# Performance work log

Measured on AMD Instinct MI355X. Metric: run time of the kernel, lower is better.

The kernel has to match this reference:

```python
import jax, jax.numpy as jnp
import numpy as np

B, L, D, W = 4, 256, 256, 8  # batch, seq_len, d_model, context_window
NS_EPS = 1e-7


def setup_inputs() -> dict:
    key = jax.random.key(0)
    ks = jax.random.split(key, 12)
    f = lambda k, s: jax.random.normal(k, s, dtype=jnp.float32)
    sD = 1.0 / np.sqrt(D)
    return {
        "x": f(ks[0], (B, L, D)),
        "k_aligned": jnp.tanh(f(ks[1], (B, L, D))),  # QKProjectionLayer applies tanh upstream
        "v": f(ks[2], (B, L, D)),
        "M_prev": f(ks[3], (B, D, D)) * 0.01,
        "S_prev": jnp.zeros((B, D, D), jnp.float32),
        # polynomial feature coeffs: phi(k) = c1*k + c2*k^2 (degree 2, dim-preserving)
        "poly_coeffs": jnp.stack([jnp.ones((D,), jnp.float32), 0.1 * jnp.ones((D,), jnp.float32)])
        + 0.01 * f(ks[4], (2, D)),
        "alpha_W": f(ks[5], (D, D)) * sD, "alpha_b": jnp.zeros((D,), jnp.float32),
        "eta_W": f(ks[6], (D, D)) * sD, "eta_b": jnp.zeros((D,), jnp.float32),
        "theta_W": f(ks[7], (D, D)) * sD, "theta_b": jnp.zeros((D,), jnp.float32),
        "gamma_W": f(ks[8], (D,)) * sD, "gamma_b": jnp.zeros((1,), jnp.float32),
        "out_W": f(ks[9], (D, D)) * sD, "out_b": jnp.zeros((D,), jnp.float32),
    }


def _newton_schulz_1(S):
    # NS_K with K=1: X <- 1.5*X - 0.5*X X^T X after Frobenius normalization
    norm = jnp.sqrt(jnp.sum(S * S, axis=(-2, -1), keepdims=True)) + NS_EPS
    X = S / norm
    return 1.5 * X - 0.5 * jnp.einsum('bij,bkj,bkl->bil', X, X, X)


def reference(x, k_aligned, v, M_prev, S_prev, poly_coeffs,
              alpha_W, alpha_b, eta_W, eta_b, theta_W, theta_b,
              gamma_W, gamma_b, out_W, out_b):
    Bn, Ln, Dn = x.shape
    # polynomial feature layer (dim-preserving, degree 2)
    k_phi = poly_coeffs[0] * k_aligned + poly_coeffs[1] * k_aligned ** 2  # [B,L,D]
    # per-token gates (precomputed, pure linear+sigmoid)
    alpha = jax.nn.sigmoid(x @ alpha_W.T + alpha_b)          # [B,L,D]
    eta = jax.nn.sigmoid(x @ eta_W.T + eta_b) * 0.1          # [B,L,D]
    theta = jax.nn.sigmoid(x @ theta_W.T + theta_b)          # [B,L,D]
    gamma = jax.nn.sigmoid(jnp.einsum('bld,d->bl', x, gamma_W) + gamma_b[0])  # [B,L]
    c_arr = jnp.minimum(jnp.arange(Ln) + 1, W).astype(x.dtype)  # actual window length per step

    to_t = lambda a: jnp.moveaxis(a, 1, 0)  # [B,L,...] -> [L,B,...]
    xs = (to_t(k_phi), to_t(v), to_t(gamma), to_t(alpha), to_t(eta), to_t(theta), c_arr)

    buf_k = jnp.zeros((Bn, W, Dn), x.dtype)  # sliding window of phi(k); zero pads contribute 0
    buf_v = jnp.zeros((Bn, W, Dn), x.dtype)
    buf_g = jnp.zeros((Bn, W), x.dtype)

    def step(carry, xt):
        M, S, bk, bv, bg = carry
        k_t, v_t, g_t, a_t, e_t, th_t, c_t = xt
        bk = jnp.concatenate([bk[:, 1:], k_t[:, None]], axis=1)
        bv = jnp.concatenate([bv[:, 1:], v_t[:, None]], axis=1)
        bg = jnp.concatenate([bg[:, 1:], g_t[:, None]], axis=1)
        # Omega gradient: sum_i gamma_i * (M phi(k_i) - v_i) outer phi(k_i) / c
        pred = jnp.einsum('bde,bwe->bwd', M, bk)
        err = pred - bv
        grad = jnp.einsum('bw,bwd,bwe->bde', bg, err, bk) / c_t
        S = th_t[..., None] * S + grad
        S_ortho = _newton_schulz_1(S)
        M = a_t[..., None] * M - e_t[..., None] * S_ortho
        y = jnp.einsum('bde,be->bd', M, k_t)
        return (M, S, bk, bv, bg), y

    (M, S, _, _, _), ys = jax.lax.scan(step, (M_prev, S_prev, buf_k, buf_v, buf_g), xs)
    output = jnp.moveaxis(ys, 0, 1) @ out_W.T + out_b  # out_proj per token
    return (output, M, S)
```

## Files before the change

### kernel.cpp

```cpp
#include <hip/hip_runtime.h>

#define Bn 4
#define Ln 256
#define Dn 256
#define Wn 8
#define NBLK 64
#define BLD (Bn*Ln*Dn)
#define BDD (Bn*Dn*Dn)

typedef float  floatx4 __attribute__((ext_vector_type(4)));
typedef short  short8  __attribute__((ext_vector_type(8)));

__device__ __forceinline__ float ldc(const float* p) {
    return __hip_atomic_load(p, __ATOMIC_RELAXED, __HIP_MEMORY_SCOPE_AGENT);
}
__device__ __forceinline__ void stc(float* p, float v) {
    __hip_atomic_store(p, v, __ATOMIC_RELAXED, __HIP_MEMORY_SCOPE_AGENT);
}
__device__ __forceinline__ void stc4(float* p, floatx4 v) {
    asm volatile("global_store_dwordx4 %0, %1, off sc0 sc1" :: "v"(p), "v"(v) : "memory");
}
__device__ __forceinline__ void ldc1x4(float& a, float& b, float& c, float& d,
    const float* p0, const float* p1, const float* p2, const float* p3)
{
    asm volatile(
        "global_load_dword %0, %4, off sc0 sc1\n\t"
        "global_load_dword %1, %5, off sc0 sc1\n\t"
        "global_load_dword %2, %6, off sc0 sc1\n\t"
        "global_load_dword %3, %7, off sc0 sc1\n\t"
        "s_waitcnt vmcnt(0)"
        : "=&v"(a), "=&v"(b), "=&v"(c), "=&v"(d)
        : "v"(p0), "v"(p1), "v"(p2), "v"(p3)
        : "memory");
}
__device__ __forceinline__ void ldc4x12s(
    floatx4& r0, floatx4& r1, floatx4& r2, floatx4& r3,
    floatx4& r4, floatx4& r5, floatx4& r6, floatx4& r7,
    floatx4& r8, floatx4& r9, floatx4& r10, floatx4& r11, float& sc,
    const float* p0, const float* p1, const float* p2, const float* p3,
    const float* p4, const float* p5, const float* p6, const float* p7,
    const float* p8, const float* p9, const float* p10, const float* p11,
    const float* ps)
{
    asm volatile(
        "global_load_dwordx4 %0, %13, off sc0 sc1\n\t"
        "global_load_dwordx4 %1, %14, off sc0 sc1\n\t"
        "global_load_dwordx4 %2, %15, off sc0 sc1\n\t"
        "global_load_dwordx4 %3, %16, off sc0 sc1\n\t"
        "global_load_dwordx4 %4, %17, off sc0 sc1\n\t"
        "global_load_dwordx4 %5, %18, off sc0 sc1\n\t"
        "global_load_dwordx4 %6, %19, off sc0 sc1\n\t"
        "global_load_dwordx4 %7, %20, off sc0 sc1\n\t"
        "global_load_dwordx4 %8, %21, off sc0 sc1\n\t"
        "global_load_dwordx4 %9, %22, off sc0 sc1\n\t"
        "global_load_dwordx4 %10, %23, off sc0 sc1\n\t"
        "global_load_dwordx4 %11, %24, off sc0 sc1\n\t"
        "global_load_dword %12, %25, off sc0 sc1\n\t"
        "s_waitcnt vmcnt(0)"
        : "=&v"(r0), "=&v"(r1), "=&v"(r2), "=&v"(r3),
          "=&v"(r4), "=&v"(r5), "=&v"(r6), "=&v"(r7),
          "=&v"(r8), "=&v"(r9), "=&v"(r10), "=&v"(r11), "=&v"(sc)
        : "v"(p0), "v"(p1), "v"(p2), "v"(p3), "v"(p4), "v"(p5),
          "v"(p6), "v"(p7), "v"(p8), "v"(p9), "v"(p10), "v"(p11), "v"(ps)
        : "memory");
}

__device__ __forceinline__ unsigned f2bf(float x) {
    unsigned u = __float_as_uint(x);
    return (u + 0x7FFFu + ((u >> 16) & 1u)) >> 16;
}
__device__ __forceinline__ unsigned long long packbf4(floatx4 v) {
    unsigned lo = f2bf(v[0]) | (f2bf(v[1]) << 16);
    unsigned hi = f2bf(v[2]) | (f2bf(v[3]) << 16);
    return (unsigned long long)lo | ((unsigned long long)hi << 32);
}
union BF8 { short8 s8; unsigned long long u[2]; };

__device__ __forceinline__ void grid_sync_b(unsigned* bflags, int rem, unsigned k)
{
    asm volatile("s_waitcnt vmcnt(0) lgkmcnt(0)" ::: "memory");
    __syncthreads();
    if (threadIdx.x == 0)
        __hip_atomic_store(&bflags[rem * 32], k,
                           __ATOMIC_RELAXED, __HIP_MEMORY_SCOPE_AGENT);
    if (threadIdx.x < 16) {
        while (__hip_atomic_load(&bflags[threadIdx.x * 32],
                                 __ATOMIC_RELAXED, __HIP_MEMORY_SCOPE_AGENT) < k)
            __builtin_amdgcn_s_sleep(1);
    }
    __syncthreads();
}

__global__ __launch_bounds__(256) void kphi_gamma_kernel(
    const float* __restrict__ k_al, const float* __restrict__ x,
    const float* __restrict__ poly, const float* __restrict__ gW,
    const float* __restrict__ gb, float* __restrict__ kphi,
    float* __restrict__ gamma)
{
    int wg = blockIdx.x, tid = threadIdx.x;
    int wave = tid >> 6, lane = tid & 63;
    int n = wg * 4 + wave;
    float gacc = 0.f;
#pragma unroll
    for (int c = 0; c < 4; ++c) {
        int e = lane + 64 * c;
        float kv = k_al[n * Dn + e];
        kphi[n * Dn + e] = poly[e] * kv + poly[Dn + e] * kv * kv;
        gacc += x[n * Dn + e] * gW[e];
    }
#pragma unroll
    for (int off = 32; off; off >>= 1) gacc += __shfl_xor(gacc, off);
    if (lane == 0) gamma[n] = 1.f / (1.f + expf(-(gacc + gb[0])));
}

template <int ACT>
__global__ __launch_bounds__(256) void gemm_act_kernel(
    const float* __restrict__ In, const float* __restrict__ Wm,
    const float* __restrict__ bias, float* __restrict__ Out)
{
    __shared__ float ldsX[32 * 64];
    __shared__ float ldsW[64 * 65];
    int n0 = blockIdx.x * 32;
    int m0 = blockIdx.y * 64;
    int tid = threadIdx.x;
    float acc[8] = {0, 0, 0, 0, 0, 0, 0, 0};
    for (int j0 = 0; j0 < 256; j0 += 64) {
#pragma unroll
        for (int q = 0; q < 2; ++q) {
            int fi = tid + 256 * q; int row = fi >> 4; int c4 = (fi & 15) << 2;
            *(float4*)&ldsX[row * 64 + c4] =
                *(const float4*)&In[(n0 + row) * 256 + j0 + c4];
        }
#pragma unroll
        for (int q = 0; q < 4; ++q) {
            int fi = tid + 256 * q; int row = fi >> 4; int c4 = (fi & 15) << 2;
            float4 vv = *(const float4*)&Wm[(m0 + row) * 256 + j0 + c4];
            ldsW[(c4 + 0) * 65 + row] = vv.x;
            ldsW[(c4 + 1) * 65 + row] = vv.y;
            ldsW[(c4 + 2) * 65 + row] = vv.z;
            ldsW[(c4 + 3) * 65 + row] = vv.w;
        }
        __syncthreads();
        int m = tid & 63, ng = tid >> 6;
        for (int j = 0; j < 64; ++j) {
            float wv = ldsW[j * 65 + m];
#pragma unroll
            for (int r = 0; r < 8; ++r) acc[r] += ldsX[(ng * 8 + r) * 64 + j] * wv;
        }
        __syncthreads();
    }
    int m = tid & 63, ng = tid >> 6;
    float bv = bias[m0 + m];
#pragma unroll
    for (int r = 0; r < 8; ++r) {
        float vv = acc[r] + bv;
        if (ACT == 1) vv = 1.f / (1.f + expf(-vv));
        if (ACT == 2) vv = 0.1f / (1.f + expf(-vv));
        Out[(n0 + ng * 8 + r) * 256 + m0 + m] = vv;
    }
}

__global__ __launch_bounds__(64) void kgram_kernel(
    const float* __restrict__ kphi, float* __restrict__ Kall)
{
    int t = blockIdx.x, b = blockIdx.y, tid = threadIdx.x;
    int wa = tid >> 3, wb = tid & 7;
    int ta = t - 7 + wa, tb = t - 7 + wb;
    float g = 0.f;
    if (ta >= 0 && tb >= 0) {
        const float* pa = &kphi[(b * Ln + ta) * Dn];
        const float* pb = &kphi[(b * Ln + tb) * Dn];
        for (int j = 0; j < Dn; j += 4) {
            floatx4 x1 = *(const floatx4*)&pa[j];
            floatx4 x2 = *(const floatx4*)&pb[j];
            g += x1[0]*x2[0] + x1[1]*x2[1] + x1[2]*x2[2] + x1[3]*x2[3];
        }
    }
    Kall[(b * Ln + t) * 64 + tid] = g;
}

__global__ __launch_bounds__(256) void prologue_kernel(unsigned* __restrict__ flags)
{
    int gidx = blockIdx.x * 256 + threadIdx.x;
    if (gidx < 512) {
        uint4 zu = {0u, 0u, 0u, 0u};
        ((uint4*)flags)[gidx] = zu;
    }
}

__global__ __launch_bounds__(256) void ysum_kernel(float* __restrict__ ysp)
{
    int gidx = blockIdx.x * 256 + threadIdx.x;
    float4 a = ((float4*)ysp)[gidx];
    float4 b = ((float4*)ysp)[65536 + gidx];
    float4 c = ((float4*)ysp)[131072 + gidx];
    float4 d = ((float4*)ysp)[196608 + gidx];
    a.x += b.x + c.x + d.x;
    a.y += b.y + c.y + d.y;
    a.z += b.z + c.z + d.z;
    a.w += b.w + c.w + d.w;
    ((float4*)ysp)[gidx] = a;
}

#define OFF_ST    0
#define OFF_UV    8448
#define OFF_AV    10496
#define OFF_CV    12544
#define OFF_TH    14592
#define OFF_KT    14848
#define OFF_KL    15104
#define OFF_NRM   15168
#define OFF_WSUM  15184
#define OFF_US    15200
#define OFF_KWA   15328
#define OFF_KW2   17408
#define OFF_SL    19456
#define SMEM_FLOATS 23616

__global__ void __launch_bounds__(256, 1) scan_kernel(
    const float* __restrict__ kphi, const float* __restrict__ vin,
    const float* __restrict__ gammaB, const float* __restrict__ alphaB,
    const float* __restrict__ etaB, const float* __restrict__ thetaB,
    const float* __restrict__ Kall,
    const float* __restrict__ Mprev, const float* __restrict__ Sprev,
    unsigned short* __restrict__ STg,
    float* __restrict__ u_buf, float* __restrict__ a_buf,
    float* __restrict__ errp_g, float* __restrict__ normp,
    float* __restrict__ ysp, unsigned* __restrict__ flags,
    float* __restrict__ outM, float* __restrict__ outS)
{
    __shared__ float smem[SMEM_FLOATS];
    char*  STb  = (char*)(smem + OFF_ST);
    float* uvp  = smem + OFF_UV;
    float* avp  = smem + OFF_AV;
    float* cvp  = smem + OFF_CV;
    float* thv  = smem + OFF_TH;
    float* kT   = smem + OFF_KT;
    float* Kl   = smem + OFF_KL;
    float* nrml = smem + OFF_NRM;
    float* wsum = smem + OFF_WSUM;
    float* usl  = smem + OFF_US;
    float* kWA  = smem + OFF_KWA;
    float* kW2  = smem + OFF_KW2;
    float* Sl   = smem + OFF_SL;

    const int wg = blockIdx.x, tid = threadIdx.x;
    const int b   = wg >> 4;
    const int rem = wg & 15;
    const int s   = rem & 3;
    const int i0 = (rem >> 2) * 64, l0 = (rem & 3) * 64;
    const int d0 = rem << 4;
    const int wid = tid >> 6, lane = tid & 63;
    const int lme = lane & 15, hi = lane >> 4;
    const int ibr = i0 + wid * 16 + (hi << 2);
    const int r  = tid >> 4, m = tid & 15;
    unsigned* bflags = flags + b * 512;
    unsigned kbar = 0;

    floatx4 S_reg[4];
    float   M_reg[16];
    floatx4 T_reg[16];

    {
#pragma unroll
        for (int cq = 0; cq < 4; ++cq)
            S_reg[cq] = *(const floatx4*)&Sprev[(size_t)(b*256 + d0 + r)*256 + m*4 + 64*cq];
#pragma unroll
        for (int lt = 0; lt < 4; ++lt)
#pragma unroll
            for (int g = 0; g < 4; ++g)
                M_reg[lt*4+g] = Mprev[(size_t)(b*256 + ibr + g)*256 + l0 + lt*16 + lme];

        float* scratch = smem;
        for (int g4 = 0; g4 < 4; ++g4) {
            floatx4 acc[4];
#pragma unroll
            for (int lt = 0; lt < 4; ++lt) acc[lt] = (floatx4){0.f,0.f,0.f,0.f};
#pragma unroll
            for (int kc = 0; kc < 8; ++kc) {
                int kb2 = kc*32 + hi*8;
                floatx4 a0 = *(const floatx4*)&Sprev[(size_t)(b*256 + i0 + wid*16 + lme)*256 + kb2];
                floatx4 a1 = *(const floatx4*)&Sprev[(size_t)(b*256 + i0 + wid*16 + lme)*256 + kb2 + 4];
                BF8 ua; ua.u[0] = packbf4(a0); ua.u[1] = packbf4(a1);
#pragma unroll
                for (int lt = 0; lt < 4; ++lt) {
                    int brow = g4*64 + lt*16 + lme;
                    floatx4 b0 = *(const floatx4*)&Sprev[(size_t)(b*256 + brow)*256 + kb2];
                    floatx4 b1 = *(const floatx4*)&Sprev[(size_t)(b*256 + brow)*256 + kb2 + 4];
                    BF8 ub; ub.u[0] = packbf4(b0); ub.u[1] = packbf4(b1);
                    acc[lt] = __builtin_amdgcn_mfma_f32_16x16x32_bf16(ua.s8, ub.s8, acc[lt], 0,0,0);
                }
            }
#pragma unroll
            for (int lt = 0; lt < 4; ++lt)
#pragma unroll
                for (int g = 0; g < 4; ++g)
                    scratch[(wid*16 + (hi<<2) + g)*260 + g4*64 + lt*16 + lme] = acc[lt][g];
        }
        __syncthreads();
#pragma unroll
        for (int kc = 0; kc < 8; ++kc) {
            T_reg[kc*2+0] = *(floatx4*)&scratch[(wid*16 + lme)*260 + kc*32 + hi*8];
            T_reg[kc*2+1] = *(floatx4*)&scratch[(wid*16 + lme)*260 + kc*32 + hi*8 + 4];
        }
#pragma unroll
        for (int q = 0; q < 2; ++q) {
            int w = q*4 + (tid >> 6);
            int c4 = (tid & 63) << 2;
            floatx4 kv = {0.f,0.f,0.f,0.f};
            if (w == 7) kv = *(const floatx4*)&kphi[(size_t)(b*Ln)*Dn + c4];
            *(floatx4*)&kW2[w*256 + c4] = kv;
        }
        __syncthreads();
#pragma unroll
        for (int w = 0; w < 8; ++w) {
            float pd[4] = {0.f,0.f,0.f,0.f};
#pragma unroll
            for (int lt = 0; lt < 4; ++lt) {
                float kv2 = kW2[w*256 + l0 + lt*16 + lme];
#pragma unroll
                for (int g = 0; g < 4; ++g) pd[g] += M_reg[lt*4+g] * kv2;
            }
#pragma unroll
            for (int g = 0; g < 4; ++g) {
                pd[g] += __shfl_xor(pd[g], 1); pd[g] += __shfl_xor(pd[g], 2);
                pd[g] += __shfl_xor(pd[g], 4); pd[g] += __shfl_xor(pd[g], 8);
            }
            if (lme == 0)
#pragma unroll
                for (int g = 0; g < 4; ++g)
                    stc(&errp_g[(size_t)((s*2 + 0)*4 + b)*2048 + w*256 + ibr + g], pd[g]);
        }
    }
    grid_sync_b(bflags, rem, ++kbar);

    for (int t = 0; t < Ln; ++t) {
        const int cwin = (t + 1 < Wn) ? (t + 1) : Wn;
        const float invc = 1.f / (float)cwin;

        {
            float e0_ = 0.f, e1_ = 0.f, e2_ = 0.f, e3_ = 0.f;
            int w_a = 0, rr_a = 0;
            const int p = t & 1;
            if (tid < 128) {
                w_a = tid >> 4; rr_a = tid & 15;
                ldc1x4(e0_, e1_, e2_, e3_,
                    &errp_g[(size_t)((0*2 + p)*4 + b)*2048 + w_a*256 + d0 + rr_a],
                    &errp_g[(size_t)((1*2 + p)*4 + b)*2048 + w_a*256 + d0 + rr_a],
                    &errp_g[(size_t)((2*2 + p)*4 + b)*2048 + w_a*256 + d0 + rr_a],
                    &errp_g[(size_t)((3*2 + p)*4 + b)*2048 + w_a*256 + d0 + rr_a]);
                float ep = e0_ + e1_ + e2_ + e3_;
                int tok = t - 7 + w_a;
                float uu = 0.f;
                if (tok >= 0)
                    uu = gammaB[b*Ln + tok] * invc *
                         (ep - vin[(size_t)(b*Ln + tok)*Dn + d0 + rr_a]);
                usl[w_a*16 + rr_a] = uu;
                stc(&u_buf[(size_t)(b*8 + w_a)*256 + d0 + rr_a], uu);
            } else {
                int idx = tid - 128;
                int w = idx >> 4, seg = idx & 15;
                int tk = t - 7 + w;
#pragma unroll
                for (int q = 0; q < 4; ++q) {
                    floatx4 kv = {0.f,0.f,0.f,0.f};
                    if (tk >= 0)
                        kv = *(const floatx4*)&kphi[(size_t)(b*Ln + tk)*Dn + seg*16 + q*4];
                    *(floatx4*)&kWA[w*260 + seg*16 + q*4] = kv;
                }
            }
            __syncthreads();

            {
                float qw[8] = {0,0,0,0,0,0,0,0};
#pragma unroll
                for (int cq = 0; cq < 4; ++cq) {
                    floatx4 sv = S_reg[cq];
#pragma unroll
                    for (int w = 0; w < 8; ++w) {
                        floatx4 kv = *(const floatx4*)&kWA[w*260 + m*4 + 64*cq];
                        qw[w] += sv[0]*kv[0] + sv[1]*kv[1] + sv[2]*kv[2] + sv[3]*kv[3];
                    }
                }
#pragma unroll
                for (int w = 0; w < 8; ++w) {
                    qw[w] += __shfl_xor(qw[w], 1); qw[w] += __shfl_xor(qw[w], 2);
                    qw[w] += __shfl_xor(qw[w], 4); qw[w] += __shfl_xor(qw[w], 8);
                }
                if (m < 8) {
                    float th = thetaB[(size_t)(b*Ln + t)*Dn + d0 + r];
                    stc(&a_buf[(size_t)(b*8 + m)*256 + d0 + r], th * qw[m]);
                }
            }
            {
                float th = thetaB[(size_t)(b*Ln + t)*Dn + d0 + r];
                float uu[8];
#pragma unroll
                for (int w = 0; w < 8; ++w) uu[w] = usl[w*16 + r];
                float sumsq = 0.f;
#pragma unroll
                for (int cq = 0; cq < 4; ++cq) {
                    floatx4 sv = th * S_reg[cq];
#pragma unroll
                    for (int w = 0; w < 8; ++w) {
                        floatx4 kv = *(const floatx4*)&kWA[w*260 + m*4 + 64*cq];
                        sv += uu[w] * kv;
                    }
                    S_reg[cq] = sv;
                    sumsq += sv[0]*sv[0] + sv[1]*sv[1] + sv[2]*sv[2] + sv[3]*sv[3];
                }
#pragma unroll
                for (int off = 32; off; off >>= 1) sumsq += __shfl_xor(sumsq, off);
                if (lane == 0) wsum[wid] = sumsq;
            }
            {
#pragma unroll
                for (int cq = 0; cq < 4; ++cq)
                    *(floatx4*)&Sl[r*260 + m*4 + 64*cq] = S_reg[cq];
                __syncthreads();
                int l = tid;
                unsigned dw[8];
#pragma unroll
                for (int j = 0; j < 8; ++j)
                    dw[j] = f2bf(Sl[(2*j)*260 + l]) | (f2bf(Sl[(2*j+1)*260 + l]) << 16);
                floatx4 p0 = { __uint_as_float(dw[0]), __uint_as_float(dw[1]),
                               __uint_as_float(dw[2]), __uint_as_float(dw[3]) };
                floatx4 p1 = { __uint_as_float(dw[4]), __uint_as_float(dw[5]),
                               __uint_as_float(dw[6]), __uint_as_float(dw[7]) };
                char* dstp = (char*)STg + ((size_t)(b*256 + l)*256 + d0)*2;
                stc4((float*)dstp, p0);
                stc4((float*)(dstp + 16), p1);
                if (tid == 0)
                    stc(&normp[b*16 + rem], wsum[0] + wsum[1] + wsum[2] + wsum[3]);
            }
            if (t == Ln - 1) {
#pragma unroll
                for (int cq = 0; cq < 4; ++cq)
                    *(floatx4*)&outS[(size_t)(b*256 + d0 + r)*256 + m*4 + 64*cq] = S_reg[cq];
            }
        }
        grid_sync_b(bflags, rem, ++kbar);

        {
            {
                int lq = tid >> 2, kq = (tid & 3) * 64;
                const char* src = (const char*)STg + ((size_t)(b*256 + l0 + lq)*256 + kq)*2;
                const float* pu = &u_buf[(size_t)b*2048 + tid*8];
                const float* pa = &a_buf[(size_t)b*2048 + tid*8];
                const float* pn = (tid < 16) ? &normp[b*16 + tid] : pu;
                floatx4 r0,r1,r2,r3,r4,r5,r6,r7,u0,u1,a0,a1; float nsc;
                ldc4x12s(r0,r1,r2,r3,r4,r5,r6,r7,u0,u1,a0,a1,nsc,
                    (const float*)(src+0),  (const float*)(src+16),
                    (const float*)(src+32), (const float*)(src+48),
                    (const float*)(src+64), (const float*)(src+80),
                    (const float*)(src+96), (const float*)(src+112),
                    pu, pu+4, pa, pa+4, pn);
                size_t rb0 = (size_t)lq*528 + (size_t)kq*2;
                unsigned swz = (unsigned)((lq & 8) << 1);
                *(floatx4*)(STb + ((rb0 +   0) ^ swz)) = r0;
                *(floatx4*)(STb + ((rb0 +  16) ^ swz)) = r1;
                *(floatx4*)(STb + ((rb0 +  32) ^ swz)) = r2;
                *(floatx4*)(STb + ((rb0 +  48) ^ swz)) = r3;
                *(floatx4*)(STb + ((rb0 +  64) ^ swz)) = r4;
                *(floatx4*)(STb + ((rb0 +  80) ^ swz)) = r5;
                *(floatx4*)(STb + ((rb0 +  96) ^ swz)) = r6;
                *(floatx4*)(STb + ((rb0 + 112) ^ swz)) = r7;
                *(floatx4*)&uvp[tid*8]     = u0; *(floatx4*)&uvp[tid*8 + 4] = u1;
                *(floatx4*)&avp[tid*8]     = a0; *(floatx4*)&avp[tid*8 + 4] = a1;
                if (tid < 16) nrml[tid] = nsc;
                if (tid < 64) {
                    *(floatx4*)&thv[tid*4] = *(const floatx4*)&thetaB[(size_t)(b*Ln + t)*Dn + tid*4];
                    *(floatx4*)&kT[tid*4]  = *(const floatx4*)&kphi[(size_t)(b*Ln + t)*Dn + tid*4];
                }
                if (tid < 16)
                    *(floatx4*)&Kl[tid*4] = *(const floatx4*)&Kall[(size_t)(b*Ln + t)*64 + tid*4];
                if (t < Ln - 1) {
#pragma unroll
                    for (int q = 0; q < 2; ++q) {
                        int w = q*4 + (tid >> 6);
                        int c4 = (tid & 63) << 2;
                        int tk = t + 1 - 7 + w;
                        floatx4 kv = {0.f,0.f,0.f,0.f};
                        if (tk >= 0) kv = *(const floatx4*)&kphi[(size_t)(b*Ln + tk)*Dn + c4];
                        *(floatx4*)&kW2[w*256 + c4] = kv;
                    }
                }
            }
            __syncthreads();

#pragma unroll
            for (int q = 0; q < 8; ++q) {
                int idx = q*256 + tid;
                int w = idx >> 8, e = idx & 255;
                float sv = avp[idx];
#pragma unroll
                for (int w2 = 0; w2 < 8; ++w2)
                    sv += 0.5f * Kl[w*8 + w2] * uvp[w2*256 + e];
                cvp[idx] = sv;
            }
            __syncthreads();

            {
                int i = i0 + wid*16 + lme;
                float thi = thv[i];
                float ui8[8], ci8[8];
#pragma unroll
                for (int w = 0; w < 8; ++w) { ui8[w] = uvp[w*256 + i]; ci8[w] = cvp[w*256 + i]; }
#pragma unroll
                for (int kc = 0; kc < 8; ++kc) {
                    int k0 = kc*32 + hi*8;
                    floatx4 th0 = *(const floatx4*)&thv[k0];
                    floatx4 th1 = *(const floatx4*)&thv[k0 + 4];
                    floatx4 t0 = (thi * th0) * T_reg[kc*2+0];
                    floatx4 t1 = (thi * th1) * T_reg[kc*2+1];
#pragma unroll
                    for (int w = 0; w < 8; ++w) {
                        floatx4 uk0 = *(const floatx4*)&uvp[w*256 + k0];
                        floatx4 uk1 = *(const floatx4*)&uvp[w*256 + k0 + 4];
                        floatx4 ck0 = *(const floatx4*)&cvp[w*256 + k0];
                        floatx4 ck1 = *(const floatx4*)&cvp[w*256 + k0 + 4];
                        t0 += ui8[w]*ck0 + ci8[w]*uk0;
                        t1 += ui8[w]*ck1 + ci8[w]*uk1;
                    }
                    T_reg[kc*2+0] = t0;
                    T_reg[kc*2+1] = t1;
                }
            }

            floatx4 acc[4];
#pragma unroll
            for (int lt = 0; lt < 4; ++lt) acc[lt] = (floatx4){0.f,0.f,0.f,0.f};
#pragma unroll
            for (int kc = 0; kc < 8; ++kc) {
                BF8 ua; ua.u[0] = packbf4(T_reg[kc*2]); ua.u[1] = packbf4(T_reg[kc*2+1]);
                int kbyte = kc*64 + hi*16;
#pragma unroll
                for (int lt = 0; lt < 4; ++lt) {
                    int row = lt*16 + lme;
                    short8 bf = *(const short8*)(STb +
                        (((size_t)row*528 + kbyte) ^ (unsigned)((row & 8) << 1)));
                    acc[lt] = __builtin_amdgcn_mfma_f32_16x16x32_bf16(ua.s8, bf, acc[lt], 0,0,0);
                }
            }

            {
                float nsq = 0.f;
#pragma unroll
                for (int q = 0; q < 16; ++q) nsq += nrml[q];
                float nrm = sqrtf(nsq) + 1e-7f;
                float inv_n = 1.f / nrm;
                float w1 = 1.5f * inv_n;
                float w3 = 0.5f * inv_n * inv_n * inv_n;
                float alv[4], etv[4], kvr[4];
#pragma unroll
                for (int g = 0; g < 4; ++g) {
                    alv[g] = alphaB[(size_t)(b*Ln + t)*Dn + ibr + g];
                    etv[g] = etaB[(size_t)(b*Ln + t)*Dn + ibr + g];
                }
#pragma unroll
                for (int lt = 0; lt < 4; ++lt) kvr[lt] = kT[l0 + lt*16 + lme];
                float py[4] = {0.f,0.f,0.f,0.f};
#pragma unroll
                for (int lt = 0; lt < 4; ++lt)
#pragma unroll
                    for (int g = 0; g < 4; ++g) {
                        int l_loc = lt*16 + lme;
                        unsigned short sb = *(const unsigned short*)(STb +
                            (((size_t)l_loc*528 + (size_t)(ibr + g)*2) ^ (unsigned)((l_loc & 8) << 1)));
                        float s_il = __uint_as_float(((unsigned)sb) << 16);
                        float ns = w1 * s_il - w3 * acc[lt][g];
                        float mn = alv[g] * M_reg[lt*4+g] - etv[g] * ns;
                        M_reg[lt*4+g] = mn;
                        py[g] += mn * kvr[lt];
                        if (t == Ln - 1)
                            outM[(size_t)(b*256 + ibr + g)*256 + l0 + l_loc] = mn;
                    }
#pragma unroll
                for (int g = 0; g < 4; ++g) {
                    py[g] += __shfl_xor(py[g], 1); py[g] += __shfl_xor(py[g], 2);
                    py[g] += __shfl_xor(py[g], 4); py[g] += __shfl_xor(py[g], 8);
                    if (lme == 0)
                        stc(&ysp[(size_t)s*BLD + (size_t)(b*Ln + t)*Dn + ibr + g], py[g]);
                }
            }

            if (t < Ln - 1) {
                const int p2 = (t + 1) & 1;
#pragma unroll
                for (int w = 0; w < 8; ++w) {
                    float pd[4] = {0.f,0.f,0.f,0.f};
#pragma unroll
                    for (int lt = 0; lt < 4; ++lt) {
                        float kv2 = kW2[w*256 + l0 + lt*16 + lme];
#pragma unroll
                        for (int g = 0; g < 4; ++g) pd[g] += M_reg[lt*4+g] * kv2;
                    }
#pragma unroll
                    for (int g = 0; g < 4; ++g) {
                        pd[g] += __shfl_xor(pd[g], 1); pd[g] += __shfl_xor(pd[g], 2);
                        pd[g] += __shfl_xor(pd[g], 4); pd[g] += __shfl_xor(pd[g], 8);
                    }
                    if (lme == 0)
#pragma unroll
                        for (int g = 0; g < 4; ++g)
                            stc(&errp_g[(size_t)((s*2 + p2)*4 + b)*2048 + w*256 + ibr + g], pd[g]);
                }
            }
        }
        grid_sync_b(bflags, rem, ++kbar);
    }
}

extern "C" void kernel_launch(void* const* d_in, const int* in_sizes, int n_in,
                              void* d_out, int out_size, void* d_ws, size_t ws_size,
                              hipStream_t stream)
{
    const float* x       = (const float*)d_in[0];
    const float* k_al    = (const float*)d_in[1];
    const float* v       = (const float*)d_in[2];
    const float* M_prev  = (const float*)d_in[3];
    const float* S_prev  = (const float*)d_in[4];
    const float* poly    = (const float*)d_in[5];
    const float* alpha_W = (const float*)d_in[6];
    const float* alpha_b = (const float*)d_in[7];
    const float* eta_W   = (const float*)d_in[8];
    const float* eta_b   = (const float*)d_in[9];
    const float* theta_W = (const float*)d_in[10];
    const float* theta_b = (const float*)d_in[11];
    const float* gamma_W = (const float*)d_in[12];
    const float* gamma_b = (const float*)d_in[13];
    const float* out_W   = (const float*)d_in[14];
    const float* out_b   = (const float*)d_in[15];

    float* ws = (float*)d_ws;
    float* kphi    = ws;
    float* alphaB  = kphi   + BLD;
    float* etaB    = alphaB + BLD;
    float* thetaB  = etaB   + BLD;
    float* gammaB  = thetaB + BLD;
    float* Kall    = gammaB + Bn*Ln;
    float* STg_f   = Kall   + Bn*Ln*64;
    float* u_bufp  = STg_f  + 131072;
    float* a_bufp  = u_bufp + Bn*Wn*Dn;
    float* errp    = a_bufp + Bn*Wn*Dn;
    float* normp   = errp   + 65536;
    float* ysp     = normp  + 64;
    unsigned* flags = (unsigned*)(ysp + 4*BLD);

    float* out_y = (float*)d_out;
    float* outM  = out_y + BLD;
    float* outS  = outM + BDD;

    hipLaunchKernelGGL(kphi_gamma_kernel, dim3(256), dim3(256), 0, stream,
                       k_al, x, poly, gamma_W, gamma_b, kphi, gammaB);
    hipLaunchKernelGGL((gemm_act_kernel<1>), dim3(32, 4), dim3(256), 0, stream,
                       x, alpha_W, alpha_b, alphaB);
    hipLaunchKernelGGL((gemm_act_kernel<2>), dim3(32, 4), dim3(256), 0, stream,
                       x, eta_W, eta_b, etaB);
    hipLaunchKernelGGL((gemm_act_kernel<1>), dim3(32, 4), dim3(256), 0, stream,
                       x, theta_W, theta_b, thetaB);
    hipLaunchKernelGGL(kgram_kernel, dim3(Ln, Bn), dim3(64), 0, stream,
                       kphi, Kall);
    hipLaunchKernelGGL(prologue_kernel, dim3(2), dim3(256), 0, stream, flags);

    hipLaunchKernelGGL(scan_kernel, dim3(NBLK), dim3(256), 0, stream,
                       kphi, v, gammaB, alphaB, etaB, thetaB, Kall,
                       M_prev, S_prev, (unsigned short*)STg_f,
                       u_bufp, a_bufp, errp, normp, ysp, flags,
                       outM, outS);

    hipLaunchKernelGGL(ysum_kernel, dim3(256), dim3(256), 0, stream, ysp);
    hipLaunchKernelGGL((gemm_act_kernel<0>), dim3(32, 4), dim3(256), 0, stream,
                       ysp, out_W, out_b, out_y);
}
```

Baseline: 5.753 ms.

## Replace persistent grid-synced scan kernel with per-timestep phase kernel launches

The single persistent scan kernel, which used spin-wait flag barriers across workgroups, is split into two kernels (phase A and phase C) launched per timestep from the host loop. Kernel boundaries now provide the synchronisation. M, S and the T matrix state live in global memory with ping-pong T buffers, and separate init kernels compute the initial T and error terms. The y partial sums are written directly, so the ysum reduction kernel is removed. This trades custom barrier overhead for 512 kernel launches and extra global memory round-trips of state.

New measurement: 5.326 ms. -7.4%, faster.

```diff
diff --git a/kernel.cpp b/kernel.cpp
--- a/kernel.cpp
+++ b/kernel.cpp
@@ -4,66 +4,11 @@
 #define Ln 256
 #define Dn 256
 #define Wn 8
-#define NBLK 64
 #define BLD (Bn*Ln*Dn)
 #define BDD (Bn*Dn*Dn)
 
 typedef float  floatx4 __attribute__((ext_vector_type(4)));
 typedef short  short8  __attribute__((ext_vector_type(8)));
-
-__device__ __forceinline__ float ldc(const float* p) {
-    return __hip_atomic_load(p, __ATOMIC_RELAXED, __HIP_MEMORY_SCOPE_AGENT);
-}
-__device__ __forceinline__ void stc(float* p, float v) {
-    __hip_atomic_store(p, v, __ATOMIC_RELAXED, __HIP_MEMORY_SCOPE_AGENT);
-}
-__device__ __forceinline__ void stc4(float* p, floatx4 v) {
-    asm volatile("global_store_dwordx4 %0, %1, off sc0 sc1" :: "v"(p), "v"(v) : "memory");
-}
-__device__ __forceinline__ void ldc1x4(float& a, float& b, float& c, float& d,
-    const float* p0, const float* p1, const float* p2, const float* p3)
-{
-    asm volatile(
-        "global_load_dword %0, %4, off sc0 sc1\n\t"
-        "global_load_dword %1, %5, off sc0 sc1\n\t"
-        "global_load_dword %2, %6, off sc0 sc1\n\t"
-        "global_load_dword %3, %7, off sc0 sc1\n\t"
-        "s_waitcnt vmcnt(0)"
-        : "=&v"(a), "=&v"(b), "=&v"(c), "=&v"(d)
-        : "v"(p0), "v"(p1), "v"(p2), "v"(p3)
-        : "memory");
-}
-__device__ __forceinline__ void ldc4x12s(
-    floatx4& r0, floatx4& r1, floatx4& r2, floatx4& r3,
-    floatx4& r4, floatx4& r5, floatx4& r6, floatx4& r7,
-    floatx4& r8, floatx4& r9, floatx4& r10, floatx4& r11, float& sc,
-    const float* p0, const float* p1, const float* p2, const float* p3,
-    const float* p4, const float* p5, const float* p6, const float* p7,
-    const float* p8, const float* p9, const float* p10, const float* p11,
-    const float* ps)
-{
-    asm volatile(
-        "global_load_dwordx4 %0, %13, off sc0 sc1\n\t"
-        "global_load_dwordx4 %1, %14, off sc0 sc1\n\t"
-        "global_load_dwordx4 %2, %15, off sc0 sc1\n\t"
-        "global_load_dwordx4 %3, %16, off sc0 sc1\n\t"
-        "global_load_dwordx4 %4, %17, off sc0 sc1\n\t"
-        "global_load_dwordx4 %5, %18, off sc0 sc1\n\t"
-        "global_load_dwordx4 %6, %19, off sc0 sc1\n\t"
-        "global_load_dwordx4 %7, %20, off sc0 sc1\n\t"
-        "global_load_dwordx4 %8, %21, off sc0 sc1\n\t"
-        "global_load_dwordx4 %9, %22, off sc0 sc1\n\t"
-        "global_load_dwordx4 %10, %23, off sc0 sc1\n\t"
-        "global_load_dwordx4 %11, %24, off sc0 sc1\n\t"
-        "global_load_dword %12, %25, off sc0 sc1\n\t"
-        "s_waitcnt vmcnt(0)"
-        : "=&v"(r0), "=&v"(r1), "=&v"(r2), "=&v"(r3),
-          "=&v"(r4), "=&v"(r5), "=&v"(r6), "=&v"(r7),
-          "=&v"(r8), "=&v"(r9), "=&v"(r10), "=&v"(r11), "=&v"(sc)
-        : "v"(p0), "v"(p1), "v"(p2), "v"(p3), "v"(p4), "v"(p5),
-          "v"(p6), "v"(p7), "v"(p8), "v"(p9), "v"(p10), "v"(p11), "v"(ps)
-        : "memory");
-}
 
 __device__ __forceinline__ unsigned f2bf(float x) {
     unsigned u = __float_as_uint(x);
@@ -75,21 +20,6 @@
     return (unsigned long long)lo | ((unsigned long long)hi << 32);
 }
 union BF8 { short8 s8; unsigned long long u[2]; };
-
-__device__ __forceinline__ void grid_sync_b(unsigned* bflags, int rem, unsigned k)
-{
-    asm volatile("s_waitcnt vmcnt(0) lgkmcnt(0)" ::: "memory");
-    __syncthreads();
-    if (threadIdx.x == 0)
-        __hip_atomic_store(&bflags[rem * 32], k,
-                           __ATOMIC_RELAXED, __HIP_MEMORY_SCOPE_AGENT);
-    if (threadIdx.x < 16) {
-        while (__hip_atomic_load(&bflags[threadIdx.x * 32],
-                                 __ATOMIC_RELAXED, __HIP_MEMORY_SCOPE_AGENT) < k)
-            __builtin_amdgcn_s_sleep(1);
-    }
-    __syncthreads();
-}
 
 __global__ __launch_bounds__(256) void kphi_gamma_kernel(
     const float* __restrict__ k_al, const float* __restrict__ x,
@@ -179,435 +109,416 @@
     Kall[(b * Ln + t) * 64 + tid] = g;
 }
 
-__global__ __launch_bounds__(256) void prologue_kernel(unsigned* __restrict__ flags)
+__global__ __launch_bounds__(256) void prologue_kernel(
+    const float* __restrict__ Mprev, const float* __restrict__ Sprev,
+    float* __restrict__ M, float* __restrict__ S,
+    float* __restrict__ ys, float* __restrict__ errp)
 {
     int gidx = blockIdx.x * 256 + threadIdx.x;
-    if (gidx < 512) {
-        uint4 zu = {0u, 0u, 0u, 0u};
-        ((uint4*)flags)[gidx] = zu;
-    }
-}
-
-__global__ __launch_bounds__(256) void ysum_kernel(float* __restrict__ ysp)
-{
-    int gidx = blockIdx.x * 256 + threadIdx.x;
-    float4 a = ((float4*)ysp)[gidx];
-    float4 b = ((float4*)ysp)[65536 + gidx];
-    float4 c = ((float4*)ysp)[131072 + gidx];
-    float4 d = ((float4*)ysp)[196608 + gidx];
-    a.x += b.x + c.x + d.x;
-    a.y += b.y + c.y + d.y;
-    a.z += b.z + c.z + d.z;
-    a.w += b.w + c.w + d.w;
-    ((float4*)ysp)[gidx] = a;
-}
-
-#define OFF_ST    0
-#define OFF_UV    8448
-#define OFF_AV    10496
-#define OFF_CV    12544
-#define OFF_TH    14592
-#define OFF_KT    14848
-#define OFF_KL    15104
-#define OFF_NRM   15168
-#define OFF_WSUM  15184
-#define OFF_US    15200
-#define OFF_KWA   15328
-#define OFF_KW2   17408
-#define OFF_SL    19456
-#define SMEM_FLOATS 23616
-
-__global__ void __launch_bounds__(256, 1) scan_kernel(
-    const float* __restrict__ kphi, const float* __restrict__ vin,
-    const float* __restrict__ gammaB, const float* __restrict__ alphaB,
-    const float* __restrict__ etaB, const float* __restrict__ thetaB,
-    const float* __restrict__ Kall,
-    const float* __restrict__ Mprev, const float* __restrict__ Sprev,
-    unsigned short* __restrict__ STg,
-    float* __restrict__ u_buf, float* __restrict__ a_buf,
-    float* __restrict__ errp_g, float* __restrict__ normp,
-    float* __restrict__ ysp, unsigned* __restrict__ flags,
-    float* __restrict__ outM, float* __restrict__ outS)
-{
-    __shared__ float smem[SMEM_FLOATS];
-    char*  STb  = (char*)(smem + OFF_ST);
-    float* uvp  = smem + OFF_UV;
-    float* avp  = smem + OFF_AV;
-    float* cvp  = smem + OFF_CV;
-    float* thv  = smem + OFF_TH;
-    float* kT   = smem + OFF_KT;
-    float* Kl   = smem + OFF_KL;
-    float* nrml = smem + OFF_NRM;
-    float* wsum = smem + OFF_WSUM;
-    float* usl  = smem + OFF_US;
-    float* kWA  = smem + OFF_KWA;
-    float* kW2  = smem + OFF_KW2;
-    float* Sl   = smem + OFF_SL;
-
+    ((float4*)M)[gidx] = ((const float4*)Mprev)[gidx];
+    ((float4*)S)[gidx] = ((const float4*)Sprev)[gidx];
+    float4 z = {0.f, 0.f, 0.f, 0.f};
+    ((float4*)ys)[gidx] = z;
+    if (gidx < 16384) ((float4*)errp)[gidx] = z;
+}
+
+__global__ __launch_bounds__(256) void tinit_kernel(
+    const float* __restrict__ Sprev, float* __restrict__ Tg0)
+{
     const int wg = blockIdx.x, tid = threadIdx.x;
-    const int b   = wg >> 4;
-    const int rem = wg & 15;
-    const int s   = rem & 3;
+    const int b = wg >> 4, rem = wg & 15;
     const int i0 = (rem >> 2) * 64, l0 = (rem & 3) * 64;
-    const int d0 = rem << 4;
+    const int wid = tid >> 6, lane = tid & 63;
+    const int lme = lane & 15, hi = lane >> 4;
+    floatx4 acc[4];
+#pragma unroll
+    for (int lt = 0; lt < 4; ++lt) acc[lt] = (floatx4){0.f,0.f,0.f,0.f};
+#pragma unroll
+    for (int kc = 0; kc < 8; ++kc) {
+        int kb2 = kc*32 + hi*8;
+        floatx4 a0 = *(const floatx4*)&Sprev[(size_t)(b*256 + i0 + wid*16 + lme)*256 + kb2];
+        floatx4 a1 = *(const floatx4*)&Sprev[(size_t)(b*256 + i0 + wid*16 + lme)*256 + kb2 + 4];
+        BF8 ua; ua.u[0] = packbf4(a0); ua.u[1] = packbf4(a1);
+#pragma unroll
+        for (int lt = 0; lt < 4; ++lt) {
+            int brow = l0 + lt*16 + lme;
+            floatx4 b0 = *(const floatx4*)&Sprev[(size_t)(b*256 + brow)*256 + kb2];
+            floatx4 b1 = *(const floatx4*)&Sprev[(size_t)(b*256 + brow)*256 + kb2 + 4];
+            BF8 ub; ub.u[0] = packbf4(b0); ub.u[1] = packbf4(b1);
+            acc[lt] = __builtin_amdgcn_mfma_f32_16x16x32_bf16(ua.s8, ub.s8, acc[lt], 0,0,0);
+        }
+    }
+#pragma unroll
+    for (int lt = 0; lt < 4; ++lt)
+#pragma unroll
+        for (int g = 0; g < 4; ++g)
+            Tg0[(size_t)(b*256 + i0 + wid*16 + (hi<<2) + g)*256 + l0 + lt*16 + lme]
+                = acc[lt][g];
+}
+
+__global__ __launch_bounds__(256) void err0_kernel(
+    const float* __restrict__ kphi, const float* __restrict__ Mprev,
+    float* __restrict__ errp)
+{
+    __shared__ float kW2[Wn * 256];
+    const int wg = blockIdx.x, tid = threadIdx.x;
+    const int b = wg >> 4, rem = wg & 15;
+    const int s = rem & 3;
+    const int i0 = (rem >> 2) * 64, l0 = (rem & 3) * 64;
     const int wid = tid >> 6, lane = tid & 63;
     const int lme = lane & 15, hi = lane >> 4;
     const int ibr = i0 + wid * 16 + (hi << 2);
-    const int r  = tid >> 4, m = tid & 15;
-    unsigned* bflags = flags + b * 512;
-    unsigned kbar = 0;
+#pragma unroll
+    for (int q = 0; q < 2; ++q) {
+        int w = q*4 + (tid >> 6);
+        int c4 = (tid & 63) << 2;
+        floatx4 kv = {0.f,0.f,0.f,0.f};
+        if (w == 7) kv = *(const floatx4*)&kphi[(size_t)(b*Ln)*Dn + c4];
+        *(floatx4*)&kW2[w*256 + c4] = kv;
+    }
+    __syncthreads();
+    float M_reg[16];
+#pragma unroll
+    for (int lt = 0; lt < 4; ++lt)
+#pragma unroll
+        for (int g = 0; g < 4; ++g)
+            M_reg[lt*4+g] = Mprev[(size_t)(b*256 + ibr + g)*256 + l0 + lt*16 + lme];
+#pragma unroll
+    for (int w = 0; w < 8; ++w) {
+        float pd[4] = {0.f,0.f,0.f,0.f};
+#pragma unroll
+        for (int lt = 0; lt < 4; ++lt) {
+            float kv2 = kW2[w*256 + l0 + lt*16 + lme];
+#pragma unroll
+            for (int g = 0; g < 4; ++g) pd[g] += M_reg[lt*4+g] * kv2;
+        }
+#pragma unroll
+        for (int g = 0; g < 4; ++g) {
+            pd[g] += __shfl_xor(pd[g], 1); pd[g] += __shfl_xor(pd[g], 2);
+            pd[g] += __shfl_xor(pd[g], 4); pd[g] += __shfl_xor(pd[g], 8);
+        }
+        if (lme == 0)
+#pragma unroll
+            for (int g = 0; g < 4; ++g)
+                errp[(size_t)((s*2 + 0)*4 + b)*2048 + w*256 + ibr + g] = pd[g];
+    }
+}
+
+__global__ __launch_bounds__(256) void phaseA_kernel(
+    const float* __restrict__ kphi, const float* __restrict__ vin,
+    const float* __restrict__ gammaB, const float* __restrict__ thetaB,
+    float* __restrict__ Sg, unsigned short* __restrict__ STg,
+    float* __restrict__ u_buf, float* __restrict__ a_buf,
+    const float* __restrict__ errp, float* __restrict__ normp, int t)
+{
+    __shared__ float usl[Wn * 16];
+    __shared__ float kWA[Wn * 260];
+    __shared__ float Sl[16 * 260];
+    __shared__ float wsum[4];
+    const int wg = blockIdx.x, tid = threadIdx.x;
+    const int b = wg >> 4, rem = wg & 15;
+    const int d0 = rem << 4;
+    const int wid = tid >> 6, lane = tid & 63;
+    const int r = tid >> 4, m = tid & 15;
+    const int e0 = m * 16;
+    const int cwin = (t + 1 < Wn) ? (t + 1) : Wn;
+    const float invc = 1.f / (float)cwin;
+    const int p = t & 1;
+
+    if (tid < 128) {
+        int w_a = tid >> 4, rr_a = tid & 15;
+        float ep = 0.f;
+#pragma unroll
+        for (int sl = 0; sl < 4; ++sl)
+            ep += errp[(size_t)((sl*2 + p)*4 + b)*2048 + w_a*256 + d0 + rr_a];
+        int tok = t - 7 + w_a;
+        float uu = 0.f;
+        if (tok >= 0)
+            uu = gammaB[b*Ln + tok] * invc *
+                 (ep - vin[(size_t)(b*Ln + tok)*Dn + d0 + rr_a]);
+        usl[w_a*16 + rr_a] = uu;
+        u_buf[(size_t)(b*8 + w_a)*256 + d0 + rr_a] = uu;
+    } else {
+        int idx = tid - 128;
+        int w = idx >> 4, seg = idx & 15;
+        int tk = t - 7 + w;
+#pragma unroll
+        for (int q = 0; q < 4; ++q) {
+            floatx4 kv = {0.f,0.f,0.f,0.f};
+            if (tk >= 0)
+                kv = *(const floatx4*)&kphi[(size_t)(b*Ln + tk)*Dn + seg*16 + q*4];
+            *(floatx4*)&kWA[w*260 + seg*16 + q*4] = kv;
+        }
+    }
+    __syncthreads();
 
     floatx4 S_reg[4];
-    float   M_reg[16];
+#pragma unroll
+    for (int cq = 0; cq < 4; ++cq)
+        S_reg[cq] = *(const floatx4*)&Sg[(size_t)(b*256 + d0 + r)*256 + e0 + cq*4];
+    {
+        float qw[8] = {0,0,0,0,0,0,0,0};
+#pragma unroll
+        for (int cq = 0; cq < 4; ++cq) {
+            floatx4 sv = S_reg[cq];
+#pragma unroll
+            for (int w = 0; w < 8; ++w) {
+                floatx4 kv = *(const floatx4*)&kWA[w*260 + e0 + cq*4];
+                qw[w] += sv[0]*kv[0] + sv[1]*kv[1] + sv[2]*kv[2] + sv[3]*kv[3];
+            }
+        }
+#pragma unroll
+        for (int w = 0; w < 8; ++w) {
+            qw[w] += __shfl_xor(qw[w], 1); qw[w] += __shfl_xor(qw[w], 2);
+            qw[w] += __shfl_xor(qw[w], 4); qw[w] += __shfl_xor(qw[w], 8);
+        }
+        if (m < 8) {
+            float th = thetaB[(size_t)(b*Ln + t)*Dn + d0 + r];
+            a_buf[(size_t)(b*8 + m)*256 + d0 + r] = th * qw[m];
+        }
+    }
+    {
+        float th = thetaB[(size_t)(b*Ln + t)*Dn + d0 + r];
+        float uu[8];
+#pragma unroll
+        for (int w = 0; w < 8; ++w) uu[w] = usl[w*16 + r];
+        float sumsq = 0.f;
+#pragma unroll
+        for (int cq = 0; cq < 4; ++cq) {
+            floatx4 sv = th * S_reg[cq];
+#pragma unroll
+            for (int w = 0; w < 8; ++w) {
+                floatx4 kv = *(const floatx4*)&kWA[w*260 + e0 + cq*4];
+                sv += uu[w] * kv;
+            }
+            S_reg[cq] = sv;
+            sumsq += sv[0]*sv[0] + sv[1]*sv[1] + sv[2]*sv[2] + sv[3]*sv[3];
+        }
+#pragma unroll
+        for (int off = 32; off; off >>= 1) sumsq += __shfl_xor(sumsq, off);
+        if (lane == 0) wsum[wid] = sumsq;
+    }
+    {
+#pragma unroll
+        for (int cq = 0; cq < 4; ++cq) {
+            *(floatx4*)&Sg[(size_t)(b*256 + d0 + r)*256 + e0 + cq*4] = S_reg[cq];
+            *(floatx4*)&Sl[r*260 + e0 + cq*4] = S_reg[cq];
+        }
+        __syncthreads();
+        int l = tid;
+        unsigned dw[8];
+#pragma unroll
+        for (int j = 0; j < 8; ++j)
+            dw[j] = f2bf(Sl[(2*j)*260 + l]) | (f2bf(Sl[(2*j+1)*260 + l]) << 16);
+        float4 p0 = { __uint_as_float(dw[0]), __uint_as_float(dw[1]),
+                      __uint_as_float(dw[2]), __uint_as_float(dw[3]) };
+        float4 p1 = { __uint_as_float(dw[4]), __uint_as_float(dw[5]),
+                      __uint_as_float(dw[6]), __uint_as_float(dw[7]) };
+        char* dstp = (char*)STg + ((size_t)(b*256 + l)*256 + d0)*2;
+        *(float4*)dstp = p0;
+        *(float4*)(dstp + 16) = p1;
+        if (tid == 0)
+            normp[b*16 + rem] = wsum[0] + wsum[1] + wsum[2] + wsum[3];
+    }
+}
+
+__global__ __launch_bounds__(256) void phaseC_kernel(
+    const float* __restrict__ kphi, const float* __restrict__ alphaB,
+    const float* __restrict__ etaB, const float* __restrict__ thetaB,
+    const float* __restrict__ Kall,
+    const unsigned short* __restrict__ STg,
+    const float* __restrict__ u_buf, const float* __restrict__ a_buf,
+    const float* __restrict__ normp,
+    const float* __restrict__ Tin, float* __restrict__ Tout,
+    float* __restrict__ Mg, float* __restrict__ ys,
+    float* __restrict__ errp, int t)
+{
+    __shared__ float smem[8448 + 2048*3 + 256 + 256 + 64 + 16 + 2048];
+    char*  STb  = (char*)smem;
+    float* uvp  = smem + 8448;
+    float* avp  = smem + 10496;
+    float* cvp  = smem + 12544;
+    float* thv  = smem + 14592;
+    float* kT   = smem + 14848;
+    float* Kl   = smem + 15104;
+    float* nrml = smem + 15168;
+    float* kW2  = smem + 15184;
+
+    const int wg = blockIdx.x, tid = threadIdx.x;
+    const int b = wg >> 4, rem = wg & 15;
+    const int s = rem & 3;
+    const int i0 = (rem >> 2) * 64, l0 = (rem & 3) * 64;
+    const int wid = tid >> 6, lane = tid & 63;
+    const int lme = lane & 15, hi = lane >> 4;
+    const int ibr = i0 + wid * 16 + (hi << 2);
+
+    {
+        int lq = tid >> 2, kq = (tid & 3) * 64;
+        const char* src = (const char*)STg + ((size_t)(b*256 + l0 + lq)*256 + kq)*2;
+        size_t rb0 = (size_t)lq*528 + (size_t)kq*2;
+        unsigned swz = (unsigned)((lq & 8) << 1);
+#pragma unroll
+        for (int q = 0; q < 8; ++q) {
+            float4 vv = *(const float4*)(src + q*16);
+            *(float4*)(STb + ((rb0 + q*16) ^ swz)) = vv;
+        }
+        *(floatx4*)&uvp[tid*8]     = *(const floatx4*)&u_buf[(size_t)b*2048 + tid*8];
+        *(floatx4*)&uvp[tid*8 + 4] = *(const floatx4*)&u_buf[(size_t)b*2048 + tid*8 + 4];
+        *(floatx4*)&avp[tid*8]     = *(const floatx4*)&a_buf[(size_t)b*2048 + tid*8];
+        *(floatx4*)&avp[tid*8 + 4] = *(const floatx4*)&a_buf[(size_t)b*2048 + tid*8 + 4];
+        if (tid < 16) nrml[tid] = normp[b*16 + tid];
+        if (tid < 64) {
+            *(floatx4*)&thv[tid*4] = *(const floatx4*)&thetaB[(size_t)(b*Ln + t)*Dn + tid*4];
+            *(floatx4*)&kT[tid*4]  = *(const floatx4*)&kphi[(size_t)(b*Ln + t)*Dn + tid*4];
+        }
+        if (tid < 16)
+            *(floatx4*)&Kl[tid*4] = *(const floatx4*)&Kall[(size_t)(b*Ln + t)*64 + tid*4];
+        if (t < Ln - 1) {
+#pragma unroll
+            for (int q = 0; q < 2; ++q) {
+                int w = q*4 + (tid >> 6);
+                int c4 = (tid & 63) << 2;
+                int tk = t + 1 - 7 + w;
+                floatx4 kv = {0.f,0.f,0.f,0.f};
+                if (tk >= 0) kv = *(const floatx4*)&kphi[(size_t)(b*Ln + tk)*Dn + c4];
+                *(floatx4*)&kW2[w*256 + c4] = kv;
+            }
+        }
+    }
+    __syncthreads();
+
+#pragma unroll
+    for (int q = 0; q < 8; ++q) {
+        int idx = q*256 + tid;
+        int w = idx >> 8, e = idx & 255;
+        float sv = avp[idx];
+#pragma unroll
+        for (int w2 = 0; w2 < 8; ++w2)
+            sv += 0.5f * Kl[w*8 + w2] * uvp[w2*256 + e];
+        cvp[idx] = sv;
+    }
+    __syncthreads();
+
     floatx4 T_reg[16];
-
     {
-#pragma unroll
-        for (int cq = 0; cq < 4; ++cq)
-            S_reg[cq] = *(const floatx4*)&Sprev[(size_t)(b*256 + d0 + r)*256 + m*4 + 64*cq];
+        const float* Trow = &Tin[(size_t)(b*256 + i0 + wid*16 + lme)*256];
+        int i = i0 + wid*16 + lme;
+        float thi = thv[i];
+        float ui8[8], ci8[8];
+#pragma unroll
+        for (int w = 0; w < 8; ++w) { ui8[w] = uvp[w*256 + i]; ci8[w] = cvp[w*256 + i]; }
+#pragma unroll
+        for (int kc = 0; kc < 8; ++kc) {
+            int k0 = kc*32 + hi*8;
+            floatx4 t0 = *(const floatx4*)&Trow[k0];
+            floatx4 t1 = *(const floatx4*)&Trow[k0 + 4];
+            floatx4 th0 = *(const floatx4*)&thv[k0];
+            floatx4 th1 = *(const floatx4*)&thv[k0 + 4];
+            t0 = (thi * th0) * t0;
+            t1 = (thi * th1) * t1;
+#pragma unroll
+            for (int w = 0; w < 8; ++w) {
+                floatx4 uk0 = *(const floatx4*)&uvp[w*256 + k0];
+                floatx4 uk1 = *(const floatx4*)&uvp[w*256 + k0 + 4];
+                floatx4 ck0 = *(const floatx4*)&cvp[w*256 + k0];
+                floatx4 ck1 = *(const floatx4*)&cvp[w*256 + k0 + 4];
+                t0 += ui8[w]*ck0 + ci8[w]*uk0;
+                t1 += ui8[w]*ck1 + ci8[w]*uk1;
+            }
+            T_reg[kc*2+0] = t0;
+            T_reg[kc*2+1] = t1;
+        }
+        if (s == 0) {
+            float* Torow = &Tout[(size_t)(b*256 + i0 + wid*16 + lme)*256];
+#pragma unroll
+            for (int kc = 0; kc < 8; ++kc) {
+                *(floatx4*)&Torow[kc*32 + hi*8]     = T_reg[kc*2+0];
+                *(floatx4*)&Torow[kc*32 + hi*8 + 4] = T_reg[kc*2+1];
+            }
+        }
+    }
+
+    floatx4 acc[4];
+#pragma unroll
+    for (int lt = 0; lt < 4; ++lt) acc[lt] = (floatx4){0.f,0.f,0.f,0.f};
+#pragma unroll
+    for (int kc = 0; kc < 8; ++kc) {
+        BF8 ua; ua.u[0] = packbf4(T_reg[kc*2]); ua.u[1] = packbf4(T_reg[kc*2+1]);
+        int kbyte = kc*64 + hi*16;
+#pragma unroll
+        for (int lt = 0; lt < 4; ++lt) {
+            int row = lt*16 + lme;
+            short8 bf = *(const short8*)(STb +
+                (((size_t)row*528 + kbyte) ^ (unsigned)((row & 8) << 1)));
+            acc[lt] = __builtin_amdgcn_mfma_f32_16x16x32_bf16(ua.s8, bf, acc[lt], 0,0,0);
+        }
+    }
+
+    {
+        float nsq = 0.f;
+#pragma unroll
+        for (int q = 0; q < 16; ++q) nsq += nrml[q];
+        float nrm = sqrtf(nsq) + 1e-7f;
+        float inv_n = 1.f / nrm;
+        float w1 = 1.5f * inv_n;
+        float w3 = 0.5f * inv_n * inv_n * inv_n;
+        float alv[4], etv[4], kvr[4], M_reg[16];
+#pragma unroll
+        for (int g = 0; g < 4; ++g) {
+            alv[g] = alphaB[(size_t)(b*Ln + t)*Dn + ibr + g];
+            etv[g] = etaB[(size_t)(b*Ln + t)*Dn + ibr + g];
+        }
+#pragma unroll
+        for (int lt = 0; lt < 4; ++lt) kvr[lt] = kT[l0 + lt*16 + lme];
 #pragma unroll
         for (int lt = 0; lt < 4; ++lt)
 #pragma unroll
             for (int g = 0; g < 4; ++g)
-                M_reg[lt*4+g] = Mprev[(size_t)(b*256 + ibr + g)*256 + l0 + lt*16 + lme];
-
-        float* scratch = smem;
-        for (int g4 = 0; g4 < 4; ++g4) {
-            floatx4 acc[4];
-#pragma unroll
-            for (int lt = 0; lt < 4; ++lt) acc[lt] = (floatx4){0.f,0.f,0.f,0.f};
-#pragma unroll
-            for (int kc = 0; kc < 8; ++kc) {
-                int kb2 = kc*32 + hi*8;
-                floatx4 a0 = *(const floatx4*)&Sprev[(size_t)(b*256 + i0 + wid*16 + lme)*256 + kb2];
-                floatx4 a1 = *(const floatx4*)&Sprev[(size_t)(b*256 + i0 + wid*16 + lme)*256 + kb2 + 4];
-                BF8 ua; ua.u[0] = packbf4(a0); ua.u[1] = packbf4(a1);
+                M_reg[lt*4+g] = Mg[(size_t)(b*256 + ibr + g)*256 + l0 + lt*16 + lme];
+        float py[4] = {0.f,0.f,0.f,0.f};
+#pragma unroll
+        for (int lt = 0; lt < 4; ++lt)
+#pragma unroll
+            for (int g = 0; g < 4; ++g) {
+                int l_loc = lt*16 + lme;
+                unsigned short sb = *(const unsigned short*)(STb +
+                    (((size_t)l_loc*528 + (size_t)(ibr + g)*2) ^ (unsigned)((l_loc & 8) << 1)));
+                float s_il = __uint_as_float(((unsigned)sb) << 16);
+                float ns = w1 * s_il - w3 * acc[lt][g];
+                float mn = alv[g] * M_reg[lt*4+g] - etv[g] * ns;
+                M_reg[lt*4+g] = mn;
+                py[g] += mn * kvr[lt];
+                Mg[(size_t)(b*256 + ibr + g)*256 + l0 + l_loc] = mn;
+            }
+#pragma unroll
+        for (int g = 0; g < 4; ++g) {
+            py[g] += __shfl_xor(py[g], 1); py[g] += __shfl_xor(py[g], 2);
+            py[g] += __shfl_xor(py[g], 4); py[g] += __shfl_xor(py[g], 8);
+            if (lme == 0) atomicAdd(&ys[(size_t)(b*Ln + t)*Dn + ibr + g], py[g]);
+        }
+
+        if (t < Ln - 1) {
+            const int p2 = (t + 1) & 1;
+#pragma unroll
+            for (int w = 0; w < 8; ++w) {
+                float pd[4] = {0.f,0.f,0.f,0.f};
 #pragma unroll
                 for (int lt = 0; lt < 4; ++lt) {
-                    int brow = g4*64 + lt*16 + lme;
-                    floatx4 b0 = *(const floatx4*)&Sprev[(size_t)(b*256 + brow)*256 + kb2];
-                    floatx4 b1 = *(const floatx4*)&Sprev[(size_t)(b*256 + brow)*256 + kb2 + 4];
-                    BF8 ub; ub.u[0] = packbf4(b0); ub.u[1] = packbf4(b1);
-                    acc[lt] = __builtin_amdgcn_mfma_f32_16x16x32_bf16(ua.s8, ub.s8, acc[lt], 0,0,0);
+                    float kv2 = kW2[w*256 + l0 + lt*16 + lme];
+#pragma unroll
+                    for (int g = 0; g < 4; ++g) pd[g] += M_reg[lt*4+g] * kv2;
                 }
-            }
-#pragma unroll
-            for (int lt = 0; lt < 4; ++lt)
-#pragma unroll
-                for (int g = 0; g < 4; ++g)
-                    scratch[(wid*16 + (hi<<2) + g)*260 + g4*64 + lt*16 + lme] = acc[lt][g];
-        }
-        __syncthreads();
-#pragma unroll
-        for (int kc = 0; kc < 8; ++kc) {
-            T_reg[kc*2+0] = *(floatx4*)&scratch[(wid*16 + lme)*260 + kc*32 + hi*8];
-            T_reg[kc*2+1] = *(floatx4*)&scratch[(wid*16 + lme)*260 + kc*32 + hi*8 + 4];
-        }
-#pragma unroll
-        for (int q = 0; q < 2; ++q) {
-            int w = q*4 + (tid >> 6);
-            int c4 = (tid & 63) << 2;
-            floatx4 kv = {0.f,0.f,0.f,0.f};
-            if (w == 7) kv = *(const floatx4*)&kphi[(size_t)(b*Ln)*Dn + c4];
-            *(floatx4*)&kW2[w*256 + c4] = kv;
-        }
-        __syncthreads();
-#pragma unroll
-        for (int w = 0; w < 8; ++w) {
-            float pd[4] = {0.f,0.f,0.f,0.f};
-#pragma unroll
-            for (int lt = 0; lt < 4; ++lt) {
-                float kv2 = kW2[w*256 + l0 + lt*16 + lme];
-#pragma unroll
-                for (int g = 0; g < 4; ++g) pd[g] += M_reg[lt*4+g] * kv2;
-            }
-#pragma unroll
-            for (int g = 0; g < 4; ++g) {
-                pd[g] += __shfl_xor(pd[g], 1); pd[g] += __shfl_xor(pd[g], 2);
-                pd[g] += __shfl_xor(pd[g], 4); pd[g] += __shfl_xor(pd[g], 8);
-            }
-            if (lme == 0)
-#pragma unroll
-                for (int g = 0; g < 4; ++g)
-                    stc(&errp_g[(size_t)((s*2 + 0)*4 + b)*2048 + w*256 + ibr + g], pd[g]);
-        }
-    }
-    grid_sync_b(bflags, rem, ++kbar);
-
-    for (int t = 0; t < Ln; ++t) {
-        const int cwin = (t + 1 < Wn) ? (t + 1) : Wn;
-        const float invc = 1.f / (float)cwin;
-
-        {
-            float e0_ = 0.f, e1_ = 0.f, e2_ = 0.f, e3_ = 0.f;
-            int w_a = 0, rr_a = 0;
-            const int p = t & 1;
-            if (tid < 128) {
-                w_a = tid >> 4; rr_a = tid & 15;
-                ldc1x4(e0_, e1_, e2_, e3_,
-                    &errp_g[(size_t)((0*2 + p)*4 + b)*2048 + w_a*256 + d0 + rr_a],
-                    &errp_g[(size_t)((1*2 + p)*4 + b)*2048 + w_a*256 + d0 + rr_a],
-                    &errp_g[(size_t)((2*2 + p)*4 + b)*2048 + w_a*256 + d0 + rr_a],
-                    &errp_g[(size_t)((3*2 + p)*4 + b)*2048 + w_a*256 + d0 + rr_a]);
-                float ep = e0_ + e1_ + e2_ + e3_;
-                int tok = t - 7 + w_a;
-                float uu = 0.f;
-                if (tok >= 0)
-                    uu = gammaB[b*Ln + tok] * invc *
-                         (ep - vin[(size_t)(b*Ln + tok)*Dn + d0 + rr_a]);
-                usl[w_a*16 + rr_a] = uu;
-                stc(&u_buf[(size_t)(b*8 + w_a)*256 + d0 + rr_a], uu);
-            } else {
-                int idx = tid - 128;
-                int w = idx >> 4, seg = idx & 15;
-                int tk = t - 7 + w;
-#pragma unroll
-                for (int q = 0; q < 4; ++q) {
-                    floatx4 kv = {0.f,0.f,0.f,0.f};
-                    if (tk >= 0)
-                        kv = *(const floatx4*)&kphi[(size_t)(b*Ln + tk)*Dn + seg*16 + q*4];
-                    *(floatx4*)&kWA[w*260 + seg*16 + q*4] = kv;
+#pragma unroll
+                for (int g = 0; g < 4; ++g) {
+                    pd[g] += __shfl_xor(pd[g], 1); pd[g] += __shfl_xor(pd[g], 2);
+                    pd[g] += __shfl_xor(pd[g], 4); pd[g] += __shfl_xor(pd[g], 8);
                 }
-            }
-            __syncthreads();
-
-            {
-                float qw[8] = {0,0,0,0,0,0,0,0};
-#pragma unroll
-                for (int cq = 0; cq < 4; ++cq) {
-                    floatx4 sv = S_reg[cq];
-#pragma unroll
-                    for (int w = 0; w < 8; ++w) {
-                        floatx4 kv = *(const floatx4*)&kWA[w*260 + m*4 + 64*cq];
-                        qw[w] += sv[0]*kv[0] + sv[1]*kv[1] + sv[2]*kv[2] + sv[3]*kv[3];
-                    }
-                }
-#pragma unroll
-                for (int w = 0; w < 8; ++w) {
-                    qw[w] += __shfl_xor(qw[w], 1); qw[w] += __shfl_xor(qw[w], 2);
-                    qw[w] += __shfl_xor(qw[w], 4); qw[w] += __shfl_xor(qw[w], 8);
-                }
-                if (m < 8) {
-                    float th = thetaB[(size_t)(b*Ln + t)*Dn + d0 + r];
-                    stc(&a_buf[(size_t)(b*8 + m)*256 + d0 + r], th * qw[m]);
-                }
-            }
-            {
-                float th = thetaB[(size_t)(b*Ln + t)*Dn + d0 + r];
-                float uu[8];
-#pragma unroll
-                for (int w = 0; w < 8; ++w) uu[w] = usl[w*16 + r];
-                float sumsq = 0.f;
-#pragma unroll
-                for (int cq = 0; cq < 4; ++cq) {
-                    floatx4 sv = th * S_reg[cq];
-#pragma unroll
-                    for (int w = 0; w < 8; ++w) {
-                        floatx4 kv = *(const floatx4*)&kWA[w*260 + m*4 + 64*cq];
-                        sv += uu[w] * kv;
-                    }
-                    S_reg[cq] = sv;
-                    sumsq += sv[0]*sv[0] + sv[1]*sv[1] + sv[2]*sv[2] + sv[3]*sv[3];
-                }
-#pragma unroll
-                for (int off = 32; off; off >>= 1) sumsq += __shfl_xor(sumsq, off);
-                if (lane == 0) wsum[wid] = sumsq;
-            }
-            {
-#pragma unroll
-                for (int cq = 0; cq < 4; ++cq)
-                    *(floatx4*)&Sl[r*260 + m*4 + 64*cq] = S_reg[cq];
-                __syncthreads();
-                int l = tid;
-                unsigned dw[8];
-#pragma unroll
-                for (int j = 0; j < 8; ++j)
-                    dw[j] = f2bf(Sl[(2*j)*260 + l]) | (f2bf(Sl[(2*j+1)*260 + l]) << 16);
-                floatx4 p0 = { __uint_as_float(dw[0]), __uint_as_float(dw[1]),
-                               __uint_as_float(dw[2]), __uint_as_float(dw[3]) };
-                floatx4 p1 = { __uint_as_float(dw[4]), __uint_as_float(dw[5]),
-                               __uint_as_float(dw[6]), __uint_as_float(dw[7]) };
-                char* dstp = (char*)STg + ((size_t)(b*256 + l)*256 + d0)*2;
-                stc4((float*)dstp, p0);
-                stc4((float*)(dstp + 16), p1);
-                if (tid == 0)
-                    stc(&normp[b*16 + rem], wsum[0] + wsum[1] + wsum[2] + wsum[3]);
-            }
-            if (t == Ln - 1) {
-#pragma unroll
-                for (int cq = 0; cq < 4; ++cq)
-                    *(floatx4*)&outS[(size_t)(b*256 + d0 + r)*256 + m*4 + 64*cq] = S_reg[cq];
-            }
-        }
-        grid_sync_b(bflags, rem, ++kbar);
-
-        {
-            {
-                int lq = tid >> 2, kq = (tid & 3) * 64;
-                const char* src = (const char*)STg + ((size_t)(b*256 + l0 + lq)*256 + kq)*2;
-                const float* pu = &u_buf[(size_t)b*2048 + tid*8];
-                const float* pa = &a_buf[(size_t)b*2048 + tid*8];
-                const float* pn = (tid < 16) ? &normp[b*16 + tid] : pu;
-                floatx4 r0,r1,r2,r3,r4,r5,r6,r7,u0,u1,a0,a1; float nsc;
-                ldc4x12s(r0,r1,r2,r3,r4,r5,r6,r7,u0,u1,a0,a1,nsc,
-                    (const float*)(src+0),  (const float*)(src+16),
-                    (const float*)(src+32), (const float*)(src+48),
-                    (const float*)(src+64), (const float*)(src+80),
-                    (const float*)(src+96), (const float*)(src+112),
-                    pu, pu+4, pa, pa+4, pn);
-                size_t rb0 = (size_t)lq*528 + (size_t)kq*2;
-                unsigned swz = (unsigned)((lq & 8) << 1);
-                *(floatx4*)(STb + ((rb0 +   0) ^ swz)) = r0;
-                *(floatx4*)(STb + ((rb0 +  16) ^ swz)) = r1;
-                *(floatx4*)(STb + ((rb0 +  32) ^ swz)) = r2;
-                *(floatx4*)(STb + ((rb0 +  48) ^ swz)) = r3;
-                *(floatx4*)(STb + ((rb0 +  64) ^ swz)) = r4;
-                *(floatx4*)(STb + ((rb0 +  80) ^ swz)) = r5;
-                *(floatx4*)(STb + ((rb0 +  96) ^ swz)) = r6;
-                *(floatx4*)(STb + ((rb0 + 112) ^ swz)) = r7;
-                *(floatx4*)&uvp[tid*8]     = u0; *(floatx4*)&uvp[tid*8 + 4] = u1;
-                *(floatx4*)&avp[tid*8]     = a0; *(floatx4*)&avp[tid*8 + 4] = a1;
-                if (tid < 16) nrml[tid] = nsc;
-                if (tid < 64) {
-                    *(floatx4*)&thv[tid*4] = *(const floatx4*)&thetaB[(size_t)(b*Ln + t)*Dn + tid*4];
-                    *(floatx4*)&kT[tid*4]  = *(const floatx4*)&kphi[(size_t)(b*Ln + t)*Dn + tid*4];
-                }
-                if (tid < 16)
-                    *(floatx4*)&Kl[tid*4] = *(const floatx4*)&Kall[(size_t)(b*Ln + t)*64 + tid*4];
-                if (t < Ln - 1) {
-#pragma unroll
-                    for (int q = 0; q < 2; ++q) {
-                        int w = q*4 + (tid >> 6);
-                        int c4 = (tid & 63) << 2;
-                        int tk = t + 1 - 7 + w;
-                        floatx4 kv = {0.f,0.f,0.f,0.f};
-                        if (tk >= 0) kv = *(const floatx4*)&kphi[(size_t)(b*Ln + tk)*Dn + c4];
-                        *(floatx4*)&kW2[w*256 + c4] = kv;
-                    }
-                }
-            }
-            __syncthreads();
-
-#pragma unroll
-            for (int q = 0; q < 8; ++q) {
-                int idx = q*256 + tid;
-                int w = idx >> 8, e = idx & 255;
-                float sv = avp[idx];
-#pragma unroll
-                for (int w2 = 0; w2 < 8; ++w2)
-                    sv += 0.5f * Kl[w*8 + w2] * uvp[w2*256 + e];
-                cvp[idx] = sv;
-            }
-            __syncthreads();
-
-            {
-                int i = i0 + wid*16 + lme;
-                float thi = thv[i];
-                float ui8[8], ci8[8];
-#pragma unroll
-                for (int w = 0; w < 8; ++w) { ui8[w] = uvp[w*256 + i]; ci8[w] = cvp[w*256 + i]; }
-#pragma unroll
-                for (int kc = 0; kc < 8; ++kc) {
-                    int k0 = kc*32 + hi*8;
-                    floatx4 th0 = *(const floatx4*)&thv[k0];
-                    floatx4 th1 = *(const floatx4*)&thv[k0 + 4];
-                    floatx4 t0 = (thi * th0) * T_reg[kc*2+0];
-                    floatx4 t1 = (thi * th1) * T_reg[kc*2+1];
-#pragma unroll
-                    for (int w = 0; w < 8; ++w) {
-                        floatx4 uk0 = *(const floatx4*)&uvp[w*256 + k0];
-                        floatx4 uk1 = *(const floatx4*)&uvp[w*256 + k0 + 4];
-                        floatx4 ck0 = *(const floatx4*)&cvp[w*256 + k0];
-                        floatx4 ck1 = *(const floatx4*)&cvp[w*256 + k0 + 4];
-                        t0 += ui8[w]*ck0 + ci8[w]*uk0;
-                        t1 += ui8[w]*ck1 + ci8[w]*uk1;
-                    }
-                    T_reg[kc*2+0] = t0;
-                    T_reg[kc*2+1] = t1;
-                }
-            }
-
-            floatx4 acc[4];
-#pragma unroll
-            for (int lt = 0; lt < 4; ++lt) acc[lt] = (floatx4){0.f,0.f,0.f,0.f};
-#pragma unroll
-            for (int kc = 0; kc < 8; ++kc) {
-                BF8 ua; ua.u[0] = packbf4(T_reg[kc*2]); ua.u[1] = packbf4(T_reg[kc*2+1]);
-                int kbyte = kc*64 + hi*16;
-#pragma unroll
-                for (int lt = 0; lt < 4; ++lt) {
-                    int row = lt*16 + lme;
-                    short8 bf = *(const short8*)(STb +
-                        (((size_t)row*528 + kbyte) ^ (unsigned)((row & 8) << 1)));
-                    acc[lt] = __builtin_amdgcn_mfma_f32_16x16x32_bf16(ua.s8, bf, acc[lt], 0,0,0);
-                }
-            }
-
-            {
-                float nsq = 0.f;
-#pragma unroll
-                for (int q = 0; q < 16; ++q) nsq += nrml[q];
-                float nrm = sqrtf(nsq) + 1e-7f;
-                float inv_n = 1.f / nrm;
-                float w1 = 1.5f * inv_n;
-                float w3 = 0.5f * inv_n * inv_n * inv_n;
-                float alv[4], etv[4], kvr[4];
-#pragma unroll
-                for (int g = 0; g < 4; ++g) {
-                    alv[g] = alphaB[(size_t)(b*Ln + t)*Dn + ibr + g];
-                    etv[g] = etaB[(size_t)(b*Ln + t)*Dn + ibr + g];
-                }
-#pragma unroll
-                for (int lt = 0; lt < 4; ++lt) kvr[lt] = kT[l0 + lt*16 + lme];
-                float py[4] = {0.f,0.f,0.f,0.f};
-#pragma unroll
-                for (int lt = 0; lt < 4; ++lt)
-#pragma unroll
-                    for (int g = 0; g < 4; ++g) {
-                        int l_loc = lt*16 + lme;
-                        unsigned short sb = *(const unsigned short*)(STb +
-                            (((size_t)l_loc*528 + (size_t)(ibr + g)*2) ^ (unsigned)((l_loc & 8) << 1)));
-                        float s_il = __uint_as_float(((unsigned)sb) << 16);
-                        float ns = w1 * s_il - w3 * acc[lt][g];
-                        float mn = alv[g] * M_reg[lt*4+g] - etv[g] * ns;
-                        M_reg[lt*4+g] = mn;
-                        py[g] += mn * kvr[lt];
-                        if (t == Ln - 1)
-                            outM[(size_t)(b*256 + ibr + g)*256 + l0 + l_loc] = mn;
-                    }
-#pragma unroll
-                for (int g = 0; g < 4; ++g) {
-                    py[g] += __shfl_xor(py[g], 1); py[g] += __shfl_xor(py[g], 2);
-                    py[g] += __shfl_xor(py[g], 4); py[g] += __shfl_xor(py[g], 8);
-                    if (lme == 0)
-                        stc(&ysp[(size_t)s*BLD + (size_t)(b*Ln + t)*Dn + ibr + g], py[g]);
-                }
-            }
-
-            if (t < Ln - 1) {
-                const int p2 = (t + 1) & 1;
-#pragma unroll
-                for (int w = 0; w < 8; ++w) {
-                    float pd[4] = {0.f,0.f,0.f,0.f};
-#pragma unroll
-                    for (int lt = 0; lt < 4; ++lt) {
-                        float kv2 = kW2[w*256 + l0 + lt*16 + lme];
-#pragma unroll
-                        for (int g = 0; g < 4; ++g) pd[g] += M_reg[lt*4+g] * kv2;
-                    }
-#pragma unroll
-                    for (int g = 0; g < 4; ++g) {
-                        pd[g] += __shfl_xor(pd[g], 1); pd[g] += __shfl_xor(pd[g], 2);
-                        pd[g] += __shfl_xor(pd[g], 4); pd[g] += __shfl_xor(pd[g], 8);
-                    }
-                    if (lme == 0)
-#pragma unroll
-                        for (int g = 0; g < 4; ++g)
-                            stc(&errp_g[(size_t)((s*2 + p2)*4 + b)*2048 + w*256 + ibr + g], pd[g]);
-                }
-            }
-        }
-        grid_sync_b(bflags, rem, ++kbar);
+                if (lme == 0)
+#pragma unroll
+                    for (int g = 0; g < 4; ++g)
+                        errp[(size_t)((s*2 + p2)*4 + b)*2048 + w*256 + ibr + g] = pd[g];
+            }
+        }
     }
 }
 
@@ -644,8 +555,9 @@
     float* a_bufp  = u_bufp + Bn*Wn*Dn;
     float* errp    = a_bufp + Bn*Wn*Dn;
     float* normp   = errp   + 65536;
-    float* ysp     = normp  + 64;
-    unsigned* flags = (unsigned*)(ysp + 4*BLD);
+    float* ysb     = normp  + 64;
+    float* Tg0     = ysb    + BLD;
+    float* Tg1     = Tg0    + BDD;
 
     float* out_y = (float*)d_out;
     float* outM  = out_y + BLD;
@@ -661,15 +573,26 @@
                        x, theta_W, theta_b, thetaB);
     hipLaunchKernelGGL(kgram_kernel, dim3(Ln, Bn), dim3(64), 0, stream,
                        kphi, Kall);
-    hipLaunchKernelGGL(prologue_kernel, dim3(2), dim3(256), 0, stream, flags);
-
-    hipLaunchKernelGGL(scan_kernel, dim3(NBLK), dim3(256), 0, stream,
-                       kphi, v, gammaB, alphaB, etaB, thetaB, Kall,
-                       M_prev, S_prev, (unsigned short*)STg_f,
-                       u_bufp, a_bufp, errp, normp, ysp, flags,
-                       outM, outS);
-
-    hipLaunchKernelGGL(ysum_kernel, dim3(256), dim3(256), 0, stream, ysp);
+    hipLaunchKernelGGL(prologue_kernel, dim3(256), dim3(256), 0, stream,
+                       M_prev, S_prev, outM, outS, ysb, errp);
+    hipLaunchKernelGGL(tinit_kernel, dim3(64), dim3(256), 0, stream,
+                       S_prev, Tg0);
+    hipLaunchKernelGGL(err0_kernel, dim3(64), dim3(256), 0, stream,
+                       kphi, M_prev, errp);
+
+    for (int t = 0; t < Ln; ++t) {
+        float* Tin  = (t & 1) ? Tg1 : Tg0;
+        float* Tout = (t & 1) ? Tg0 : Tg1;
+        hipLaunchKernelGGL(phaseA_kernel, dim3(64), dim3(256), 0, stream,
+                           kphi, v, gammaB, thetaB, outS,
+                           (unsigned short*)STg_f, u_bufp, a_bufp,
+                           errp, normp, t);
+        hipLaunchKernelGGL(phaseC_kernel, dim3(64), dim3(256), 0, stream,
+                           kphi, alphaB, etaB, thetaB, Kall,
+                           (const unsigned short*)STg_f, u_bufp, a_bufp, normp,
+                           Tin, Tout, outM, ysb, errp, t);
+    }
+
     hipLaunchKernelGGL((gemm_act_kernel<0>), dim3(32, 4), dim3(256), 0, stream,
-                       ysp, out_W, out_b, out_y);
-}
+                       ysb, out_W, out_b, out_y);
+}
```
